# Kernel tuning notes

Hardware: AMD Instinct MI355X
Metric: run time of the kernel (lower is better)

The kernel has to match this reference:

```python
import jax, jax.numpy as jnp
import numpy as np

NEG_INF = -1e9


def setup_inputs() -> dict:
    key = jax.random.key(0)
    ks = jax.random.split(key, 6)
    B, S, ENC, DEC = 32, 2048, 1024, 1024
    decoder_hidden = jax.random.normal(ks[0], (B, DEC), dtype=jnp.float32)
    encoder_outputs = jax.random.normal(ks[1], (B, S, ENC), dtype=jnp.float32)
    mask = jax.random.randint(ks[2], (B, S), 0, 2, dtype=jnp.int32)
    # nn.Linear-style weights, scaled ~ 1/sqrt(fan_in)
    W_h = jax.random.normal(ks[3], (DEC, ENC), dtype=jnp.float32) / np.sqrt(ENC)
    W_s = jax.random.normal(ks[4], (DEC, DEC), dtype=jnp.float32) / np.sqrt(DEC)
    v = jax.random.normal(ks[5], (DEC,), dtype=jnp.float32) / np.sqrt(DEC)
    return {
        "decoder_hidden": decoder_hidden,
        "encoder_outputs": encoder_outputs,
        "mask": mask,
        "W_h": W_h,
        "W_s": W_s,
        "v": v,
    }


def reference(decoder_hidden, encoder_outputs, mask, W_h, W_s, v):
    # dec: [B, D] -> [B, 1, D]
    dec = jnp.einsum("bd,ed->be", decoder_hidden, W_s)[:, None, :]
    # enc: [B, S, E] -> [B, S, D]
    enc = jnp.einsum("bse,de->bsd", encoder_outputs, W_h)
    # energy: [B, S] via rank-1 projection with v
    energy = jnp.einsum("bsd,d->bs", jnp.tanh(enc + dec), v)
    energy = jnp.where(mask == 0, NEG_INF, energy)
    attn_weights = jax.nn.softmax(energy, axis=1)  # [B, S]
    # context: [B, E]
    context = jnp.einsum("bs,bse->be", attn_weights, encoder_outputs)
    return (context, attn_weights)
```

## Files before the change

kernel.cpp:

```cpp
#include <hip/hip_runtime.h>
#include <stdint.h>
#include <math.h>

typedef __attribute__((ext_vector_type(8))) short short8;
typedef __attribute__((ext_vector_type(4))) float f32x4;

#define S_LEN 2048
#define NBATCH 32
#define KDIM 1024
#define NEG_INF_F (-1e9f)

#define BM 256
#define BN 256

__device__ __forceinline__ uint32_t pack_bf16(float f0, float f1) {
    union { float f; uint32_t u; } a, b; a.f = f0; b.f = f1;
    return ((a.u + 0x8000u) >> 16) | ((b.u + 0x8000u) & 0xFFFF0000u);
}

__device__ __forceinline__ void gload_lds16(const unsigned short* g, unsigned short* l) {
    __builtin_amdgcn_global_load_lds(
        (const __attribute__((address_space(1))) void*)g,
        (__attribute__((address_space(3))) void*)l, 16, 0, 0);
}

__device__ __forceinline__ float fast_tanh(float x) {
    float e = __expf(2.0f * x);
    return 1.0f - 2.0f * __builtin_amdgcn_rcpf(e + 1.0f);
}

__global__ __launch_bounds__(256) void dec_kernel(
    const float* __restrict__ dh, const float* __restrict__ Ws,
    float* __restrict__ dec)
{
    __shared__ float wrow[1024];
    int e = blockIdx.x;
    int t = threadIdx.x;
    #pragma unroll
    for (int i = t; i < 1024; i += 256) wrow[i] = Ws[(size_t)e * 1024 + i];
    __syncthreads();
    int b = t >> 3, part = t & 7;
    const float* dhp = dh + (size_t)b * 1024 + part * 128;
    const float* wp  = wrow + part * 128;
    float s = 0.f;
    #pragma unroll 8
    for (int i = 0; i < 128; ++i) s += dhp[i] * wp[i];
    s += __shfl_xor(s, 1);
    s += __shfl_xor(s, 2);
    s += __shfl_xor(s, 4);
    if (part == 0) dec[(size_t)b * 1024 + e] = s;
}

__global__ __launch_bounds__(256) void convert_frag_B(
    const float* __restrict__ src, unsigned short* __restrict__ out)
{
    int gid = blockIdx.x * 4 + (threadIdx.x >> 6);
    int lane = threadIdx.x & 63;
    int ms = gid & 63, ks = gid >> 6;
    const float* p = src + (size_t)(ms * 16 + (lane & 15)) * 1024
                         + ks * 32 + (lane >> 4) * 8;
    f32x4 a = *(const f32x4*)p;
    f32x4 b = *(const f32x4*)(p + 4);
    union { uint32_t d[4]; short8 v; } o;
    o.d[0] = pack_bf16(a.x, a.y); o.d[1] = pack_bf16(a.z, a.w);
    o.d[2] = pack_bf16(b.x, b.y); o.d[3] = pack_bf16(b.z, b.w);
    *(short8*)(out + (size_t)gid * 512 + lane * 8) = o.v;
}

__global__ __launch_bounds__(256) void convert_frag_A(
    const float* __restrict__ src, unsigned short* __restrict__ out)
{
    int gid = blockIdx.x * 4 + (threadIdx.x >> 6);
    int lane = threadIdx.x & 63;
    int ms = gid >> 5, ks = gid & 31;
    const float* p = src + (size_t)(ms * 16 + (lane & 15)) * 1024
                         + ks * 32 + (lane >> 4) * 8;
    f32x4 a = *(const f32x4*)p;
    f32x4 b = *(const f32x4*)(p + 4);
    union { uint32_t d[4]; short8 v; } o;
    o.d[0] = pack_bf16(a.x, a.y); o.d[1] = pack_bf16(a.z, a.w);
    o.d[2] = pack_bf16(b.x, b.y); o.d[3] = pack_bf16(b.z, b.w);
    *(short8*)(out + ((size_t)ks * 4096 + ms) * 512 + lane * 8) = o.v;
}

__global__ __launch_bounds__(512, 2) void energy_gemm_v9(
    const unsigned short* __restrict__ Ahi,
    const unsigned short* __restrict__ Bhi,
    const float* __restrict__ dec, const float* __restrict__ v,
    float* __restrict__ energy)
{
    __shared__ unsigned short lds[65536];

    int bid = blockIdx.x;
    int lid = (bid & 7) * 128 + (bid >> 3);
    int mblk = lid >> 2, nblk = lid & 3;
    int m0 = mblk * BM, n0 = nblk * BN;
    int b = m0 >> 11;

    int t = threadIdx.x, wid = t >> 6, lane = t & 63;
    int wm = wid >> 2, wn = wid & 3;
    int kg = lane >> 4, lr = lane & 15;

    f32x4 acc[8][4] = {};

    auto stage = [&](int t2, unsigned short* buf) {
        #pragma unroll
        for (int i = 0; i < 4; ++i) {
            int c = wid * 4 + i;
            int ks = 2 * t2 + (c >> 4);
            gload_lds16(Ahi + ((size_t)ks * 4096 + mblk * 16 + (c & 15)) * 512 + lane * 8,
                        &buf[c * 512]);
        }
        #pragma unroll
        for (int i = 0; i < 4; ++i) {
            int c = wid * 4 + i;
            int ks = 2 * t2 + (c >> 4);
            gload_lds16(Bhi + ((size_t)ks * 64 + nblk * 16 + (c & 15)) * 512 + lane * 8,
                        &buf[16384 + c * 512]);
        }
    };

    stage(0, &lds[0]);
    asm volatile("s_waitcnt vmcnt(0)" ::: "memory");
    __builtin_amdgcn_s_barrier();

    for (int ts = 0; ts < 16; ++ts) {
        unsigned short* bufA = &lds[(ts & 1) * 32768];
        unsigned short* bufB = bufA + 16384;

        if (ts < 15) stage(ts + 1, &lds[((ts + 1) & 1) * 32768]);

        #pragma unroll
        for (int ksl = 0; ksl < 2; ++ksl) {
            short8 bf[4];
            #pragma unroll
            for (int ni = 0; ni < 4; ++ni)
                bf[ni] = *(const short8*)&bufB[(ksl * 16 + wn * 4 + ni) * 512 + lane * 8];
            #pragma unroll
            for (int mi = 0; mi < 8; ++mi) {
                short8 af = *(const short8*)&bufA[(ksl * 16 + wm * 8 + mi) * 512 + lane * 8];
                #pragma unroll
                for (int ni = 0; ni < 4; ++ni)
                    acc[mi][ni] = __builtin_amdgcn_mfma_f32_16x16x32_bf16(af, bf[ni], acc[mi][ni], 0, 0, 0);
            }
        }

        asm volatile("s_waitcnt vmcnt(0)" ::: "memory");
        __builtin_amdgcn_s_barrier();
    }

    float vv[4], dd[4];
    #pragma unroll
    for (int ni = 0; ni < 4; ++ni) {
        int d = n0 + wn * 64 + ni * 16 + lr;
        vv[ni] = v[d];
        dd[ni] = dec[(size_t)b * 1024 + d];
    }
    #pragma unroll
    for (int mi = 0; mi < 8; ++mi) {
        #pragma unroll
        for (int r = 0; r < 4; ++r) {
            float local = 0.f;
            #pragma unroll
            for (int ni = 0; ni < 4; ++ni)
                local += fast_tanh(acc[mi][ni][r] + dd[ni]) * vv[ni];
            local += __shfl_xor(local, 1);
            local += __shfl_xor(local, 2);
            local += __shfl_xor(local, 4);
            local += __shfl_xor(local, 8);
            if (lr == 0) {
                int m = m0 + wm * 128 + mi * 16 + kg * 4 + r;
                atomicAdd(&energy[m], local);
            }
        }
    }
}

__global__ __launch_bounds__(256) void softmax_kernel(
    const float* __restrict__ energy, const int* __restrict__ mask,
    float* __restrict__ attn)
{
    int b = blockIdx.x;
    int t = threadIdx.x;
    int wid = t >> 6, lane = t & 63;
    __shared__ float wmax[4], wsum[4];

    float vals[8];
    float mx = -INFINITY;
    #pragma unroll
    for (int j = 0; j < 8; ++j) {
        int s = t + j * 256;
        float e = energy[(size_t)b * S_LEN + s];
        if (mask[(size_t)b * S_LEN + s] == 0) e = NEG_INF_F;
        vals[j] = e;
        mx = fmaxf(mx, e);
    }
    #pragma unroll
    for (int m = 1; m < 64; m <<= 1) mx = fmaxf(mx, __shfl_xor(mx, m));
    if (lane == 0) wmax[wid] = mx;
    __syncthreads();
    mx = fmaxf(fmaxf(wmax[0], wmax[1]), fmaxf(wmax[2], wmax[3]));

    float sum = 0.f;
    #pragma unroll
    for (int j = 0; j < 8; ++j) { vals[j] = expf(vals[j] - mx); sum += vals[j]; }
    #pragma unroll
    for (int m = 1; m < 64; m <<= 1) sum += __shfl_xor(sum, m);
    if (lane == 0) wsum[wid] = sum;
    __syncthreads();
    sum = wsum[0] + wsum[1] + wsum[2] + wsum[3];
    float inv = 1.f / sum;
    #pragma unroll
    for (int j = 0; j < 8; ++j)
        attn[(size_t)b * S_LEN + t + j * 256] = vals[j] * inv;
}

__global__ __launch_bounds__(256) void context_kernel(
    const float* __restrict__ attn, const float* __restrict__ x,
    float* __restrict__ ctx)
{
    int ec = blockIdx.x, b = blockIdx.y, sc = blockIdx.z;
    int e = ec * 256 + threadIdx.x;
    const float* xp = x + ((size_t)b * S_LEN + sc * 128) * KDIM + e;
    const float* ap = attn + (size_t)b * S_LEN + sc * 128;
    float acc = 0.f;
    #pragma unroll 4
    for (int s = 0; s < 128; ++s) acc += ap[s] * xp[(size_t)s * KDIM];
    atomicAdd(&ctx[(size_t)b * KDIM + e], acc);
}

extern "C" void kernel_launch(void* const* d_in, const int* in_sizes, int n_in,
                              void* d_out, int out_size, void* d_ws, size_t ws_size,
                              hipStream_t stream) {
    const float* dh   = (const float*)d_in[0];
    const float* x    = (const float*)d_in[1];
    const int*   mask = (const int*)d_in[2];
    const float* Wh   = (const float*)d_in[3];
    const float* Ws   = (const float*)d_in[4];
    const float* v    = (const float*)d_in[5];

    float* ctx  = (float*)d_out;
    float* attn = (float*)d_out + 32 * 1024;

    unsigned short* Ahi = (unsigned short*)d_ws;
    unsigned short* Bhi = Ahi + 67108864ull;
    float* dec    = (float*)(Bhi + 1048576ull);
    float* energy = dec + 32768;

    hipMemsetAsync(energy, 0, 65536 * sizeof(float), stream);
    hipMemsetAsync(ctx, 0, 32768 * sizeof(float), stream);

    dec_kernel<<<1024, 256, 0, stream>>>(dh, Ws, dec);
    convert_frag_B<<<512, 256, 0, stream>>>(Wh, Bhi);
    convert_frag_A<<<32768, 256, 0, stream>>>(x, Ahi);
    energy_gemm_v9<<<1024, 512, 0, stream>>>(Ahi, Bhi, dec, v, energy);
    softmax_kernel<<<NBATCH, 256, 0, stream>>>(energy, mask, attn);
    context_kernel<<<dim3(4, NBATCH, 16), 256, 0, stream>>>(attn, x, ctx);
}
```

Measured before the change: 288.7 us.

## Fuse fp32-to-bf16 conversion of encoder outputs into the energy GEMM A-tile load

```diff
diff --git a/kernel.cpp b/kernel.cpp
--- a/kernel.cpp
+++ b/kernel.cpp
@@ -12,6 +12,7 @@
 
 #define BM 256
 #define BN 256
+#define LDA 72
 
 __device__ __forceinline__ uint32_t pack_bf16(float f0, float f1) {
     union { float f; uint32_t u; } a, b; a.f = f0; b.f = f1;
@@ -67,29 +68,13 @@
     *(short8*)(out + (size_t)gid * 512 + lane * 8) = o.v;
 }
 
-__global__ __launch_bounds__(256) void convert_frag_A(
-    const float* __restrict__ src, unsigned short* __restrict__ out)
-{
-    int gid = blockIdx.x * 4 + (threadIdx.x >> 6);
-    int lane = threadIdx.x & 63;
-    int ms = gid >> 5, ks = gid & 31;
-    const float* p = src + (size_t)(ms * 16 + (lane & 15)) * 1024
-                         + ks * 32 + (lane >> 4) * 8;
-    f32x4 a = *(const f32x4*)p;
-    f32x4 b = *(const f32x4*)(p + 4);
-    union { uint32_t d[4]; short8 v; } o;
-    o.d[0] = pack_bf16(a.x, a.y); o.d[1] = pack_bf16(a.z, a.w);
-    o.d[2] = pack_bf16(b.x, b.y); o.d[3] = pack_bf16(b.z, b.w);
-    *(short8*)(out + ((size_t)ks * 4096 + ms) * 512 + lane * 8) = o.v;
-}
-
-__global__ __launch_bounds__(512, 2) void energy_gemm_v9(
-    const unsigned short* __restrict__ Ahi,
+__global__ __launch_bounds__(512, 2) void energy_gemm_v10(
+    const float* __restrict__ x,
     const unsigned short* __restrict__ Bhi,
     const float* __restrict__ dec, const float* __restrict__ v,
     float* __restrict__ energy)
 {
-    __shared__ unsigned short lds[65536];
+    __shared__ unsigned short lds[69632];
 
     int bid = blockIdx.x;
     int lid = (bid & 7) * 128 + (bid >> 3);
@@ -103,49 +88,79 @@
 
     f32x4 acc[8][4] = {};
 
-    auto stage = [&](int t2, unsigned short* buf) {
-        #pragma unroll
-        for (int i = 0; i < 4; ++i) {
-            int c = wid * 4 + i;
-            int ks = 2 * t2 + (c >> 4);
-            gload_lds16(Ahi + ((size_t)ks * 4096 + mblk * 16 + (c & 15)) * 512 + lane * 8,
-                        &buf[c * 512]);
-        }
+    int arow = t >> 1, acg = t & 1;
+    const float* aptr = x + (size_t)(m0 + arow) * KDIM + acg * 16;
+    int awoff = arow * LDA + acg * 16;
+
+    f32x4 A0, A1, A2, A3;
+
+    auto stageB = [&](int t2, unsigned short* bufB) {
         #pragma unroll
         for (int i = 0; i < 4; ++i) {
             int c = wid * 4 + i;
             int ks = 2 * t2 + (c >> 4);
             gload_lds16(Bhi + ((size_t)ks * 64 + nblk * 16 + (c & 15)) * 512 + lane * 8,
-                        &buf[16384 + c * 512]);
+                        &bufB[c * 512]);
         }
     };
 
-    stage(0, &lds[0]);
-    asm volatile("s_waitcnt vmcnt(0)" ::: "memory");
+#define A_LOAD(t2, bb) { \
+    const float* ap_ = aptr + (t2) * 64 + (bb) * 32; \
+    A0 = *(const f32x4*)ap_;        A1 = *(const f32x4*)(ap_ + 4); \
+    A2 = *(const f32x4*)(ap_ + 8);  A3 = *(const f32x4*)(ap_ + 12); }
+#define A_WRITE(bufA, bb) { \
+    union { uint32_t d[8]; } o_; \
+    o_.d[0] = pack_bf16(A0.x, A0.y); o_.d[1] = pack_bf16(A0.z, A0.w); \
+    o_.d[2] = pack_bf16(A1.x, A1.y); o_.d[3] = pack_bf16(A1.z, A1.w); \
+    o_.d[4] = pack_bf16(A2.x, A2.y); o_.d[5] = pack_bf16(A2.z, A2.w); \
+    o_.d[6] = pack_bf16(A3.x, A3.y); o_.d[7] = pack_bf16(A3.z, A3.w); \
+    *(short8*)&(bufA)[awoff + (bb) * 32]     = *(short8*)&o_.d[0]; \
+    *(short8*)&(bufA)[awoff + (bb) * 32 + 8] = *(short8*)&o_.d[4]; }
+
+#define KSLOT(bufA, bufB, ksl) { \
+    short8 bf[4]; \
+    _Pragma("unroll") \
+    for (int ni = 0; ni < 4; ++ni) \
+        bf[ni] = *(const short8*)&(bufB)[((ksl) * 16 + wn * 4 + ni) * 512 + lane * 8]; \
+    _Pragma("unroll") \
+    for (int mi = 0; mi < 8; ++mi) { \
+        short8 af = *(const short8*)&(bufA)[(wm * 128 + mi * 16 + lr) * LDA + (ksl) * 32 + kg * 8]; \
+        _Pragma("unroll") \
+        for (int ni = 0; ni < 4; ++ni) \
+            acc[mi][ni] = __builtin_amdgcn_mfma_f32_16x16x32_bf16(af, bf[ni], acc[mi][ni], 0, 0, 0); \
+    } }
+
+    {
+        unsigned short* bufA = &lds[0];
+        stageB(0, &lds[18432]);
+        A_LOAD(0, 0); A_WRITE(bufA, 0);
+        A_LOAD(0, 1); A_WRITE(bufA, 1);
+    }
+    asm volatile("s_waitcnt vmcnt(0) lgkmcnt(0)" ::: "memory");
     __builtin_amdgcn_s_barrier();
 
     for (int ts = 0; ts < 16; ++ts) {
-        unsigned short* bufA = &lds[(ts & 1) * 32768];
-        unsigned short* bufB = bufA + 16384;
-
-        if (ts < 15) stage(ts + 1, &lds[((ts + 1) & 1) * 32768]);
-
-        #pragma unroll
-        for (int ksl = 0; ksl < 2; ++ksl) {
-            short8 bf[4];
-            #pragma unroll
-            for (int ni = 0; ni < 4; ++ni)
-                bf[ni] = *(const short8*)&bufB[(ksl * 16 + wn * 4 + ni) * 512 + lane * 8];
-            #pragma unroll
-            for (int mi = 0; mi < 8; ++mi) {
-                short8 af = *(const short8*)&bufA[(ksl * 16 + wm * 8 + mi) * 512 + lane * 8];
-                #pragma unroll
-                for (int ni = 0; ni < 4; ++ni)
-                    acc[mi][ni] = __builtin_amdgcn_mfma_f32_16x16x32_bf16(af, bf[ni], acc[mi][ni], 0, 0, 0);
-            }
+        unsigned short* bufA = &lds[(ts & 1) * 34816];
+        unsigned short* bufB = bufA + 18432;
+        unsigned short* nbufA = &lds[((ts + 1) & 1) * 34816];
+        unsigned short* nbufB = nbufA + 18432;
+        const bool st = (ts < 15);
+
+        if (st) {
+            stageB(ts + 1, nbufB);
+            A_LOAD(ts + 1, 0);
+            KSLOT(bufA, bufB, 0);
+            A_WRITE(nbufA, 0);
+            __builtin_amdgcn_sched_barrier(0);
+            A_LOAD(ts + 1, 1);
+            KSLOT(bufA, bufB, 1);
+            A_WRITE(nbufA, 1);
+        } else {
+            KSLOT(bufA, bufB, 0);
+            KSLOT(bufA, bufB, 1);
         }
 
-        asm volatile("s_waitcnt vmcnt(0)" ::: "memory");
+        asm volatile("s_waitcnt vmcnt(0) lgkmcnt(0)" ::: "memory");
         __builtin_amdgcn_s_barrier();
     }
 
@@ -242,8 +257,7 @@
     float* ctx  = (float*)d_out;
     float* attn = (float*)d_out + 32 * 1024;
 
-    unsigned short* Ahi = (unsigned short*)d_ws;
-    unsigned short* Bhi = Ahi + 67108864ull;
+    unsigned short* Bhi = (unsigned short*)d_ws;
     float* dec    = (float*)(Bhi + 1048576ull);
     float* energy = dec + 32768;
 
@@ -252,8 +266,7 @@
 
     dec_kernel<<<1024, 256, 0, stream>>>(dh, Ws, dec);
     convert_frag_B<<<512, 256, 0, stream>>>(Wh, Bhi);
-    convert_frag_A<<<32768, 256, 0, stream>>>(x, Ahi);
-    energy_gemm_v9<<<1024, 512, 0, stream>>>(Ahi, Bhi, dec, v, energy);
+    energy_gemm_v10<<<1024, 512, 0, stream>>>(x, Bhi, dec, v, energy);
     softmax_kernel<<<NBATCH, 256, 0, stream>>>(energy, mask, attn);
     context_kernel<<<dim3(4, NBATCH, 16), 256, 0, stream>>>(attn, x, ctx);
 }
```

New measurement: 263.2 us, median of 3. 8.8% less time.

## Restructure energy GEMM main loop into 4-stage LDS ring with interleaved MFMA

Applied to the files above, without the earlier changes.

```diff
diff --git a/kernel.cpp b/kernel.cpp
--- a/kernel.cpp
+++ b/kernel.cpp
@@ -83,7 +83,7 @@
     *(short8*)(out + ((size_t)ks * 4096 + ms) * 512 + lane * 8) = o.v;
 }
 
-__global__ __launch_bounds__(512, 2) void energy_gemm_v9(
+__global__ __launch_bounds__(512, 2) void energy_gemm_v13(
     const unsigned short* __restrict__ Ahi,
     const unsigned short* __restrict__ Bhi,
     const float* __restrict__ dec, const float* __restrict__ v,
@@ -103,49 +103,66 @@
 
     f32x4 acc[8][4] = {};
 
-    auto stage = [&](int t2, unsigned short* buf) {
-        #pragma unroll
-        for (int i = 0; i < 4; ++i) {
+    auto stageHalf2 = [&](int h2, int i0) {
+        unsigned short* dst = &lds[(h2 & 3) * 16384];
+        #pragma unroll
+        for (int i = i0; i < i0 + 2; ++i) {
             int c = wid * 4 + i;
-            int ks = 2 * t2 + (c >> 4);
-            gload_lds16(Ahi + ((size_t)ks * 4096 + mblk * 16 + (c & 15)) * 512 + lane * 8,
-                        &buf[c * 512]);
-        }
-        #pragma unroll
-        for (int i = 0; i < 4; ++i) {
-            int c = wid * 4 + i;
-            int ks = 2 * t2 + (c >> 4);
-            gload_lds16(Bhi + ((size_t)ks * 64 + nblk * 16 + (c & 15)) * 512 + lane * 8,
-                        &buf[16384 + c * 512]);
+            const unsigned short* g = (c < 16)
+                ? Ahi + ((size_t)h2 * 4096 + mblk * 16 + c) * 512
+                : Bhi + ((size_t)h2 * 64 + nblk * 16 + (c - 16)) * 512;
+            gload_lds16(g + lane * 8, &dst[c * 512]);
         }
     };
 
-    stage(0, &lds[0]);
-    asm volatile("s_waitcnt vmcnt(0)" ::: "memory");
+    stageHalf2(0, 0); stageHalf2(0, 2);
+    stageHalf2(1, 0); stageHalf2(1, 2);
+    stageHalf2(2, 0); stageHalf2(2, 2);
+    asm volatile("s_waitcnt vmcnt(8)" ::: "memory");
     __builtin_amdgcn_s_barrier();
 
-    for (int ts = 0; ts < 16; ++ts) {
-        unsigned short* bufA = &lds[(ts & 1) * 32768];
-        unsigned short* bufB = bufA + 16384;
-
-        if (ts < 15) stage(ts + 1, &lds[((ts + 1) & 1) * 32768]);
-
-        #pragma unroll
-        for (int ksl = 0; ksl < 2; ++ksl) {
-            short8 bf[4];
+    for (int hg = 0; hg < 32; ++hg) {
+        unsigned short* base = &lds[(hg & 3) * 16384];
+        const bool st = (hg < 29);
+
+        short8 bf[4], af[4];
+
+        #pragma unroll
+        for (int ni = 0; ni < 4; ++ni)
+            bf[ni] = *(const short8*)&base[8192 + (wn * 4 + ni) * 512 + lane * 8];
+        #pragma unroll
+        for (int j = 0; j < 4; ++j)
+            af[j] = *(const short8*)&base[(wm * 8 + j) * 512 + lane * 8];
+        if (st) stageHalf2(hg + 3, 0);
+        __builtin_amdgcn_s_barrier();
+        asm volatile("s_waitcnt lgkmcnt(0)" ::: "memory");
+        __builtin_amdgcn_sched_barrier(0);
+        __builtin_amdgcn_s_setprio(1);
+        #pragma unroll
+        for (int j = 0; j < 4; ++j)
             #pragma unroll
             for (int ni = 0; ni < 4; ++ni)
-                bf[ni] = *(const short8*)&bufB[(ksl * 16 + wn * 4 + ni) * 512 + lane * 8];
+                acc[j][ni] = __builtin_amdgcn_mfma_f32_16x16x32_bf16(af[j], bf[ni], acc[j][ni], 0, 0, 0);
+        __builtin_amdgcn_s_setprio(0);
+        __builtin_amdgcn_s_barrier();
+
+        #pragma unroll
+        for (int j = 0; j < 4; ++j)
+            af[j] = *(const short8*)&base[(wm * 8 + 4 + j) * 512 + lane * 8];
+        if (st) stageHalf2(hg + 3, 2);
+        __builtin_amdgcn_s_barrier();
+        asm volatile("s_waitcnt lgkmcnt(0)" ::: "memory");
+        __builtin_amdgcn_sched_barrier(0);
+        __builtin_amdgcn_s_setprio(1);
+        #pragma unroll
+        for (int j = 0; j < 4; ++j)
             #pragma unroll
-            for (int mi = 0; mi < 8; ++mi) {
-                short8 af = *(const short8*)&bufA[(ksl * 16 + wm * 8 + mi) * 512 + lane * 8];
-                #pragma unroll
-                for (int ni = 0; ni < 4; ++ni)
-                    acc[mi][ni] = __builtin_amdgcn_mfma_f32_16x16x32_bf16(af, bf[ni], acc[mi][ni], 0, 0, 0);
-            }
-        }
-
-        asm volatile("s_waitcnt vmcnt(0)" ::: "memory");
+            for (int ni = 0; ni < 4; ++ni)
+                acc[4 + j][ni] = __builtin_amdgcn_mfma_f32_16x16x32_bf16(af[j], bf[ni], acc[4 + j][ni], 0, 0, 0);
+        __builtin_amdgcn_s_setprio(0);
+        if (st)             asm volatile("s_waitcnt vmcnt(8)" ::: "memory");
+        else if (hg == 29)  asm volatile("s_waitcnt vmcnt(4)" ::: "memory");
+        else if (hg == 30)  asm volatile("s_waitcnt vmcnt(0)" ::: "memory");
         __builtin_amdgcn_s_barrier();
     }
 
@@ -253,7 +270,7 @@
     dec_kernel<<<1024, 256, 0, stream>>>(dh, Ws, dec);
     convert_frag_B<<<512, 256, 0, stream>>>(Wh, Bhi);
     convert_frag_A<<<32768, 256, 0, stream>>>(x, Ahi);
-    energy_gemm_v9<<<1024, 512, 0, stream>>>(Ahi, Bhi, dec, v, energy);
+    energy_gemm_v13<<<1024, 512, 0, stream>>>(Ahi, Bhi, dec, v, energy);
     softmax_kernel<<<NBATCH, 256, 0, stream>>>(energy, mask, attn);
     context_kernel<<<dim3(4, NBATCH, 16), 256, 0, stream>>>(attn, x, ctx);
 }
```

Result: slower. 309.0 us (+7.0%).
